# Performance work log

Hardware: AMD Instinct MI355X
Metric: run time of the kernel (lower is better)

The kernel has to match this reference:

```python
import jax, jax.numpy as jnp
import numpy as np

G, N, E, K, D = 32768, 128, 1024, 32, 3
B = G // 2


def setup_inputs() -> dict:
    key = jax.random.key(0)
    ks = jax.random.split(key, 12)
    x = jax.random.normal(ks[0], (G, N, D), dtype=jnp.float32)
    edge_src = jax.random.randint(ks[1], (G, E), 0, N, dtype=jnp.int32)
    edge_dst = jax.random.randint(ks[2], (G, E), 0, N, dtype=jnp.int32)
    ext_x = jax.random.normal(ks[3], (G, K, D), dtype=jnp.float32)
    # xavier-normal-ish 3x3 params
    s = float(np.sqrt(2.0 / (D + D)))
    W = jax.random.normal(ks[4], (D, D), dtype=jnp.float32) * s
    M = jax.random.normal(ks[5], (D, D), dtype=jnp.float32) * s
    U = jax.random.normal(ks[6], (D, D), dtype=jnp.float32) * s
    V = jax.random.normal(ks[7], (D, D), dtype=jnp.float32) * s
    # link-prediction MLP (Linear(6,3), Linear(3,2))
    W1 = jax.random.uniform(ks[8], (2 * D, D), dtype=jnp.float32, minval=-1, maxval=1) / np.sqrt(2 * D)
    b1 = jnp.zeros((D,), dtype=jnp.float32)
    W2 = jax.random.uniform(ks[9], (D, 2), dtype=jnp.float32, minval=-1, maxval=1) / np.sqrt(D)
    b2 = jnp.zeros((2,), dtype=jnp.float32)
    return {"x": x, "edge_src": edge_src, "edge_dst": edge_dst, "ext_x": ext_x,
            "W": W, "M": M, "U": U, "V": V, "W1": W1, "b1": b1, "W2": W2, "b2": b2}


def _neigh_sum(xg, src, dst):
    # gather source node reps and scatter-add into destination nodes: [N, D]
    return jax.ops.segment_sum(xg[src], dst, num_segments=N)


def reference(x, edge_src, edge_dst, ext_x, W, M, U, V, W1, b1, W2, b2):
    # InternalGraphConvolutionLayer: h = relu(x@W + (sum of neighbour reps)@M)
    agg = jax.vmap(_neigh_sum)(x, edge_src, edge_dst)          # [G, N, D]
    h = jax.nn.relu(jnp.einsum('gnd,de->gne', x, W) +
                    jnp.einsum('gnd,de->gne', agg, M))          # [G, N, D]
    emb = jax.nn.softmax(h.sum(axis=1), axis=-1)                # [G, D]
    # ExternalGraphConvolutionLayer: relu(emb@U + sum_k ext_x@V), softmax
    ext = jax.nn.relu(emb @ U + ext_x.sum(axis=1) @ V)          # [G, D]
    g_emb = jax.nn.softmax(ext, axis=-1)                        # [G, D]
    # LinkPredictionLayer on graph pairs
    e1, e2 = g_emb[:B], g_emb[B:]                               # [B, D] each
    t = jnp.concatenate([e1 * e2, e1 + e2], axis=1)             # [B, 2D]
    hlp = jax.nn.relu(t @ W1 + b1)                              # [B, D]
    out = jax.nn.softmax(hlp @ W2 + b2, axis=-1)                # [B, 2]
    return out
```

## Files before the change

kernel.cpp:

```cpp
#include <hip/hip_runtime.h>

#define NG    32768
#define NN    128
#define NE    1024
#define NK    32
#define NB    (NG / 2)
#define RSTR  17
#define AWDW  (NN * RSTR)

__global__ __launch_bounds__(256) void dcnn_adj_kernel(
    const float* __restrict__ x,
    const int*   __restrict__ esrc,
    const int*   __restrict__ edst,
    const float* __restrict__ extx,
    const float* __restrict__ W,
    const float* __restrict__ M,
    const float* __restrict__ U,
    const float* __restrict__ V,
    const float* __restrict__ W1,
    const float* __restrict__ b1,
    const float* __restrict__ W2,
    const float* __restrict__ b2,
    float* __restrict__ out)
{
    __shared__ unsigned A[4 * AWDW];
    __shared__ float ge[4][3];

    const int t    = threadIdx.x;
    const int w    = t >> 6;
    const int lane = t & 63;
    const int pair = blockIdx.x * 2 + (w >> 1);
    const int g    = (w & 1) ? (pair + NB) : pair;

    const int gu = __builtin_amdgcn_readfirstlane(g);

    const float* __restrict__ xg = x + (size_t)gu * (NN * 3);

    const int4* sp = (const int4*)(esrc + (size_t)gu * NE);
    const int4* dp = (const int4*)(edst + (size_t)gu * NE);
    const int4 s0 = sp[lane], s1 = sp[lane + 64], s2 = sp[lane + 128], s3 = sp[lane + 192];
    const int4 d0 = dp[lane], d1 = dp[lane + 64], d2 = dp[lane + 128], d3 = dp[lane + 192];

    float er0 = 0.f, er1 = 0.f, er2 = 0.f;
    if (lane < NK) {
        const float* ep = extx + (size_t)gu * (NK * 3) + lane * 3;
        er0 = ep[0]; er1 = ep[1]; er2 = ep[2];
    }

    unsigned* Aw = &A[w * AWDW];
    #pragma unroll
    for (int i = 0; i < 34; ++i) {
        const int idx = i * 64 + lane;
        if (idx < AWDW) Aw[idx] = 0u;
    }

    __builtin_amdgcn_wave_barrier();

    #define SCAT(SV, DV)                                                    \
        {                                                                   \
            const unsigned off = (unsigned)(size_t)&Aw[(DV) * RSTR + ((SV) >> 3)]; \
            const unsigned val = 1u << (4 * ((SV) & 7));                    \
            asm volatile("ds_add_u32 %0, %1" :: "v"(off), "v"(val) : "memory"); \
        }
    SCAT(s0.x, d0.x) SCAT(s0.y, d0.y) SCAT(s0.z, d0.z) SCAT(s0.w, d0.w)
    SCAT(s1.x, d1.x) SCAT(s1.y, d1.y) SCAT(s1.z, d1.z) SCAT(s1.w, d1.w)
    SCAT(s2.x, d2.x) SCAT(s2.y, d2.y) SCAT(s2.z, d2.z) SCAT(s2.w, d2.w)
    SCAT(s3.x, d3.x) SCAT(s3.y, d3.y) SCAT(s3.z, d3.z) SCAT(s3.w, d3.w)
    #undef SCAT

    asm volatile("s_waitcnt lgkmcnt(0)" ::: "memory");
    __builtin_amdgcn_wave_barrier();

    float ac0 = 0.f, ac1 = 0.f, ac2 = 0.f;
    float ac3 = 0.f, ac4 = 0.f, ac5 = 0.f;
    const int r0 = lane * RSTR;
    const int r1 = (lane + 64) * RSTR;

    #pragma unroll
    for (int j = 0; j < 16; ++j) {
        const unsigned da = Aw[r0 + j];
        const unsigned db = Aw[r1 + j];
        float q[24];
        *(float4*)&q[0]  = *(const float4*)(xg + j * 24);
        *(float4*)&q[4]  = *(const float4*)(xg + j * 24 + 4);
        *(float4*)&q[8]  = *(const float4*)(xg + j * 24 + 8);
        *(float4*)&q[12] = *(const float4*)(xg + j * 24 + 12);
        *(float4*)&q[16] = *(const float4*)(xg + j * 24 + 16);
        *(float4*)&q[20] = *(const float4*)(xg + j * 24 + 20);
        #pragma unroll
        for (int o = 0; o < 8; ++o) {
            const float ca = (float)((da >> (4 * o)) & 15u);
            const float cb = (float)((db >> (4 * o)) & 15u);
            const float xs0 = q[o * 3], xs1 = q[o * 3 + 1], xs2 = q[o * 3 + 2];
            ac0 += ca * xs0; ac1 += ca * xs1; ac2 += ca * xs2;
            ac3 += cb * xs0; ac4 += cb * xs1; ac5 += cb * xs2;
        }
    }

    float h0, h1, h2;
    {
        const float* xr = xg + lane * 3;
        const float x0 = xr[0], x1 = xr[1], x2 = xr[2];
        h0 = fmaxf(x0 * W[0] + x1 * W[3] + x2 * W[6] +
                   ac0 * M[0] + ac1 * M[3] + ac2 * M[6], 0.f);
        h1 = fmaxf(x0 * W[1] + x1 * W[4] + x2 * W[7] +
                   ac0 * M[1] + ac1 * M[4] + ac2 * M[7], 0.f);
        h2 = fmaxf(x0 * W[2] + x1 * W[5] + x2 * W[8] +
                   ac0 * M[2] + ac1 * M[5] + ac2 * M[8], 0.f);
    }
    {
        const float* xr = xg + (lane + 64) * 3;
        const float x0 = xr[0], x1 = xr[1], x2 = xr[2];
        h0 += fmaxf(x0 * W[0] + x1 * W[3] + x2 * W[6] +
                    ac3 * M[0] + ac4 * M[3] + ac5 * M[6], 0.f);
        h1 += fmaxf(x0 * W[1] + x1 * W[4] + x2 * W[7] +
                    ac3 * M[1] + ac4 * M[4] + ac5 * M[7], 0.f);
        h2 += fmaxf(x0 * W[2] + x1 * W[5] + x2 * W[8] +
                    ac3 * M[2] + ac4 * M[5] + ac5 * M[8], 0.f);
    }

    #pragma unroll
    for (int off = 16; off > 0; off >>= 1) {
        h0  += __shfl_xor(h0,  off);
        h1  += __shfl_xor(h1,  off);
        h2  += __shfl_xor(h2,  off);
        er0 += __shfl_xor(er0, off);
        er1 += __shfl_xor(er1, off);
        er2 += __shfl_xor(er2, off);
    }
    #define RL(v) (__uint_as_float(__builtin_amdgcn_readlane(__float_as_uint(v), 0)) + \
                   __uint_as_float(__builtin_amdgcn_readlane(__float_as_uint(v), 32)))
    const float H0 = RL(h0), H1 = RL(h1), H2 = RL(h2);
    const float E0 = RL(er0), E1 = RL(er1), E2 = RL(er2);
    #undef RL

    if (lane == 0) {
        const float mx = fmaxf(H0, fmaxf(H1, H2));
        const float e0 = __expf(H0 - mx), e1 = __expf(H1 - mx), e2 = __expf(H2 - mx);
        const float inv = 1.0f / (e0 + e1 + e2);
        const float emb0 = e0 * inv, emb1 = e1 * inv, emb2 = e2 * inv;

        float ext[3];
        #pragma unroll
        for (int e = 0; e < 3; ++e) {
            const float vv = emb0 * U[e] + emb1 * U[3 + e] + emb2 * U[6 + e]
                           + E0   * V[e] + E1   * V[3 + e] + E2   * V[6 + e];
            ext[e] = fmaxf(vv, 0.f);
        }
        const float mx2 = fmaxf(ext[0], fmaxf(ext[1], ext[2]));
        const float f0 = __expf(ext[0] - mx2), f1 = __expf(ext[1] - mx2), f2 = __expf(ext[2] - mx2);
        const float inv2 = 1.0f / (f0 + f1 + f2);
        ge[w][0] = f0 * inv2; ge[w][1] = f1 * inv2; ge[w][2] = f2 * inv2;
    }

    __syncthreads();

    if ((w & 1) == 0 && lane == 0) {
        float tt[6];
        tt[0] = ge[w][0] * ge[w + 1][0];
        tt[1] = ge[w][1] * ge[w + 1][1];
        tt[2] = ge[w][2] * ge[w + 1][2];
        tt[3] = ge[w][0] + ge[w + 1][0];
        tt[4] = ge[w][1] + ge[w + 1][1];
        tt[5] = ge[w][2] + ge[w + 1][2];

        float hl[3];
        #pragma unroll
        for (int j = 0; j < 3; ++j) {
            float vv = b1[j];
            #pragma unroll
            for (int i = 0; i < 6; ++i) vv += tt[i] * W1[i * 3 + j];
            hl[j] = fmaxf(vv, 0.f);
        }

        const float l0 = b2[0] + hl[0] * W2[0] + hl[1] * W2[2] + hl[2] * W2[4];
        const float l1 = b2[1] + hl[0] * W2[1] + hl[1] * W2[3] + hl[2] * W2[5];
        const float mm = fmaxf(l0, l1);
        const float q0 = __expf(l0 - mm), q1 = __expf(l1 - mm);
        const float qi = 1.0f / (q0 + q1);
        out[(size_t)pair * 2    ] = q0 * qi;
        out[(size_t)pair * 2 + 1] = q1 * qi;
    }
}

extern "C" void kernel_launch(void* const* d_in, const int* in_sizes, int n_in,
                              void* d_out, int out_size, void* d_ws, size_t ws_size,
                              hipStream_t stream) {
    const float* x    = (const float*)d_in[0];
    const int*   esrc = (const int*)  d_in[1];
    const int*   edst = (const int*)  d_in[2];
    const float* extx = (const float*)d_in[3];
    const float* W    = (const float*)d_in[4];
    const float* M    = (const float*)d_in[5];
    const float* U    = (const float*)d_in[6];
    const float* V    = (const float*)d_in[7];
    const float* W1   = (const float*)d_in[8];
    const float* b1   = (const float*)d_in[9];
    const float* W2   = (const float*)d_in[10];
    const float* b2   = (const float*)d_in[11];
    float* out = (float*)d_out;

    dcnn_adj_kernel<<<NB / 2, 256, 0, stream>>>(
        x, esrc, edst, extx, W, M, U, V, W1, b1, W2, b2, out);
}
```

Baseline: 377.5 us.

## Split each graph across two waves with shared adjacency and block-level reduction

Each graph is now handled by two waves instead of one. Each wave scatters half the edges into a shared per-graph adjacency tile and aggregates 64 node rows instead of 128. A block now covers one graph pair, so the grid doubles. Partial sums are combined through shared memory with added __syncthreads, and launch bounds request 8 blocks per CU. This shortens per-wave serial work and LDS per block to raise parallelism, at the cost of block-wide barriers and redundant x loads across the two waves.

```diff
diff --git a/kernel.cpp b/kernel.cpp
--- a/kernel.cpp
+++ b/kernel.cpp
@@ -8,7 +8,7 @@
 #define RSTR  17
 #define AWDW  (NN * RSTR)
 
-__global__ __launch_bounds__(256) void dcnn_adj_kernel(
+__global__ __launch_bounds__(256, 8) void dcnn_adj_kernel(
     const float* __restrict__ x,
     const int*   __restrict__ esrc,
     const int*   __restrict__ edst,
@@ -23,39 +23,38 @@
     const float* __restrict__ b2,
     float* __restrict__ out)
 {
-    __shared__ unsigned A[4 * AWDW];
-    __shared__ float ge[4][3];
-
-    const int t    = threadIdx.x;
-    const int w    = t >> 6;
-    const int lane = t & 63;
-    const int pair = blockIdx.x * 2 + (w >> 1);
-    const int g    = (w & 1) ? (pair + NB) : pair;
+    __shared__ unsigned A[2 * AWDW];
+    __shared__ float pw[4][6];
+    __shared__ float ge[2][3];
+
+    const int t     = threadIdx.x;
+    const int w     = t >> 6;
+    const int lane  = t & 63;
+    const int half  = w & 1;
+    const int gslot = w >> 1;
+    const int pair  = blockIdx.x;
+    const int g     = gslot ? (pair + NB) : pair;
 
     const int gu = __builtin_amdgcn_readfirstlane(g);
-
     const float* __restrict__ xg = x + (size_t)gu * (NN * 3);
 
     const int4* sp = (const int4*)(esrc + (size_t)gu * NE);
     const int4* dp = (const int4*)(edst + (size_t)gu * NE);
-    const int4 s0 = sp[lane], s1 = sp[lane + 64], s2 = sp[lane + 128], s3 = sp[lane + 192];
-    const int4 d0 = dp[lane], d1 = dp[lane + 64], d2 = dp[lane + 128], d3 = dp[lane + 192];
+    const int ebase = half * 128 + lane;
+    const int4 s0 = sp[ebase], s1 = sp[ebase + 64];
+    const int4 d0 = dp[ebase], d1 = dp[ebase + 64];
 
     float er0 = 0.f, er1 = 0.f, er2 = 0.f;
-    if (lane < NK) {
+    if (half == 0 && lane < NK) {
         const float* ep = extx + (size_t)gu * (NK * 3) + lane * 3;
         er0 = ep[0]; er1 = ep[1]; er2 = ep[2];
     }
 
-    unsigned* Aw = &A[w * AWDW];
     #pragma unroll
-    for (int i = 0; i < 34; ++i) {
-        const int idx = i * 64 + lane;
-        if (idx < AWDW) Aw[idx] = 0u;
-    }
-
-    __builtin_amdgcn_wave_barrier();
-
+    for (int i = 0; i < 17; ++i) A[i * 256 + t] = 0u;
+    __syncthreads();
+
+    unsigned* Aw = &A[gslot * AWDW];
     #define SCAT(SV, DV)                                                    \
         {                                                                   \
             const unsigned off = (unsigned)(size_t)&Aw[(DV) * RSTR + ((SV) >> 3)]; \
@@ -64,22 +63,18 @@
         }
     SCAT(s0.x, d0.x) SCAT(s0.y, d0.y) SCAT(s0.z, d0.z) SCAT(s0.w, d0.w)
     SCAT(s1.x, d1.x) SCAT(s1.y, d1.y) SCAT(s1.z, d1.z) SCAT(s1.w, d1.w)
-    SCAT(s2.x, d2.x) SCAT(s2.y, d2.y) SCAT(s2.z, d2.z) SCAT(s2.w, d2.w)
-    SCAT(s3.x, d3.x) SCAT(s3.y, d3.y) SCAT(s3.z, d3.z) SCAT(s3.w, d3.w)
     #undef SCAT
 
     asm volatile("s_waitcnt lgkmcnt(0)" ::: "memory");
-    __builtin_amdgcn_wave_barrier();
-
+    __syncthreads();
+
+    const int row = half * 64 + lane;
+    const int r0  = row * RSTR;
     float ac0 = 0.f, ac1 = 0.f, ac2 = 0.f;
-    float ac3 = 0.f, ac4 = 0.f, ac5 = 0.f;
-    const int r0 = lane * RSTR;
-    const int r1 = (lane + 64) * RSTR;
 
     #pragma unroll
     for (int j = 0; j < 16; ++j) {
         const unsigned da = Aw[r0 + j];
-        const unsigned db = Aw[r1 + j];
         float q[24];
         *(float4*)&q[0]  = *(const float4*)(xg + j * 24);
         *(float4*)&q[4]  = *(const float4*)(xg + j * 24 + 4);
@@ -90,16 +85,15 @@
         #pragma unroll
         for (int o = 0; o < 8; ++o) {
             const float ca = (float)((da >> (4 * o)) & 15u);
-            const float cb = (float)((db >> (4 * o)) & 15u);
-            const float xs0 = q[o * 3], xs1 = q[o * 3 + 1], xs2 = q[o * 3 + 2];
-            ac0 += ca * xs0; ac1 += ca * xs1; ac2 += ca * xs2;
-            ac3 += cb * xs0; ac4 += cb * xs1; ac5 += cb * xs2;
+            ac0 += ca * q[o * 3];
+            ac1 += ca * q[o * 3 + 1];
+            ac2 += ca * q[o * 3 + 2];
         }
     }
 
     float h0, h1, h2;
     {
-        const float* xr = xg + lane * 3;
+        const float* xr = xg + row * 3;
         const float x0 = xr[0], x1 = xr[1], x2 = xr[2];
         h0 = fmaxf(x0 * W[0] + x1 * W[3] + x2 * W[6] +
                    ac0 * M[0] + ac1 * M[3] + ac2 * M[6], 0.f);
@@ -107,16 +101,6 @@
                    ac0 * M[1] + ac1 * M[4] + ac2 * M[7], 0.f);
         h2 = fmaxf(x0 * W[2] + x1 * W[5] + x2 * W[8] +
                    ac0 * M[2] + ac1 * M[5] + ac2 * M[8], 0.f);
-    }
-    {
-        const float* xr = xg + (lane + 64) * 3;
-        const float x0 = xr[0], x1 = xr[1], x2 = xr[2];
-        h0 += fmaxf(x0 * W[0] + x1 * W[3] + x2 * W[6] +
-                    ac3 * M[0] + ac4 * M[3] + ac5 * M[6], 0.f);
-        h1 += fmaxf(x0 * W[1] + x1 * W[4] + x2 * W[7] +
-                    ac3 * M[1] + ac4 * M[4] + ac5 * M[7], 0.f);
-        h2 += fmaxf(x0 * W[2] + x1 * W[5] + x2 * W[8] +
-                    ac3 * M[2] + ac4 * M[5] + ac5 * M[8], 0.f);
     }
 
     #pragma unroll
@@ -130,11 +114,22 @@
     }
     #define RL(v) (__uint_as_float(__builtin_amdgcn_readlane(__float_as_uint(v), 0)) + \
                    __uint_as_float(__builtin_amdgcn_readlane(__float_as_uint(v), 32)))
-    const float H0 = RL(h0), H1 = RL(h1), H2 = RL(h2);
-    const float E0 = RL(er0), E1 = RL(er1), E2 = RL(er2);
+    if (lane == 0) {
+        pw[w][0] = RL(h0);  pw[w][1] = RL(h1);  pw[w][2] = RL(h2);
+        pw[w][3] = RL(er0); pw[w][4] = RL(er1); pw[w][5] = RL(er2);
+    }
     #undef RL
 
-    if (lane == 0) {
+    __syncthreads();
+
+    if (half == 0 && lane == 0) {
+        const float H0 = pw[w][0] + pw[w + 1][0];
+        const float H1 = pw[w][1] + pw[w + 1][1];
+        const float H2 = pw[w][2] + pw[w + 1][2];
+        const float E0 = pw[w][3] + pw[w + 1][3];
+        const float E1 = pw[w][4] + pw[w + 1][4];
+        const float E2 = pw[w][5] + pw[w + 1][5];
+
         const float mx = fmaxf(H0, fmaxf(H1, H2));
         const float e0 = __expf(H0 - mx), e1 = __expf(H1 - mx), e2 = __expf(H2 - mx);
         const float inv = 1.0f / (e0 + e1 + e2);
@@ -150,19 +145,19 @@
         const float mx2 = fmaxf(ext[0], fmaxf(ext[1], ext[2]));
         const float f0 = __expf(ext[0] - mx2), f1 = __expf(ext[1] - mx2), f2 = __expf(ext[2] - mx2);
         const float inv2 = 1.0f / (f0 + f1 + f2);
-        ge[w][0] = f0 * inv2; ge[w][1] = f1 * inv2; ge[w][2] = f2 * inv2;
-    }
-
-    __syncthreads();
-
-    if ((w & 1) == 0 && lane == 0) {
+        ge[gslot][0] = f0 * inv2; ge[gslot][1] = f1 * inv2; ge[gslot][2] = f2 * inv2;
+    }
+
+    __syncthreads();
+
+    if (t == 0) {
         float tt[6];
-        tt[0] = ge[w][0] * ge[w + 1][0];
-        tt[1] = ge[w][1] * ge[w + 1][1];
-        tt[2] = ge[w][2] * ge[w + 1][2];
-        tt[3] = ge[w][0] + ge[w + 1][0];
-        tt[4] = ge[w][1] + ge[w + 1][1];
-        tt[5] = ge[w][2] + ge[w + 1][2];
+        tt[0] = ge[0][0] * ge[1][0];
+        tt[1] = ge[0][1] * ge[1][1];
+        tt[2] = ge[0][2] * ge[1][2];
+        tt[3] = ge[0][0] + ge[1][0];
+        tt[4] = ge[0][1] + ge[1][1];
+        tt[5] = ge[0][2] + ge[1][2];
 
         float hl[3];
         #pragma unroll
@@ -200,6 +195,6 @@
     const float* b2   = (const float*)d_in[11];
     float* out = (float*)d_out;
 
-    dcnn_adj_kernel<<<NB / 2, 256, 0, stream>>>(
+    dcnn_adj_kernel<<<NB, 256, 0, stream>>>(
         x, esrc, edst, extx, W, M, U, V, W1, b1, W2, b2, out);
 }
```

Measured after the change: 388.5 us. +2.9%, slower.
